# Kernel tuning notes

Hardware: AMD Instinct MI355X
Metric: run time of the kernel (lower is better)

Reference implementation:

```python
import jax, jax.numpy as jnp
import numpy as np

B = 4096        # args.batch_size
M = 2           # n_views (and m in approximate_hsic_zy)
N = B * M       # total rows after torch.cat of views
D = 128         # projector feature dim
GAMMA = 3.0     # args.gamma
SIGMA = 1.0     # Gaussian kernel bandwidth used by compute_gaussian_kernel


def setup_inputs() -> dict:
    key = jax.random.key(0)
    x = jax.random.normal(key, (N, D), dtype=jnp.float32)
    # module applies l2_norm (F.normalize dim=1) before hsic_objective
    feat = x / jnp.maximum(jnp.linalg.norm(x, axis=1, keepdims=True), 1e-12)
    return {"feat": feat}


def _gaussian_kernel(x, y):
    # pairwise squared distances via the GEMM trick, then Gaussian kernel
    sq = (jnp.sum(x * x, axis=1)[:, None]
          + jnp.sum(y * y, axis=1)[None, :]
          - 2.0 * (x @ y.T))
    sq = jnp.maximum(sq, 0.0)
    return jnp.exp(-sq / (2.0 * SIGMA * SIGMA))


def _approximate_hsic_zy(K):
    # labels = cat([arange(B)]*M); labels-equality matrix; exclude diagonal.
    lab = jnp.tile(jnp.arange(B), M)                      # [N]
    eq = (lab[:, None] == lab[None, :]).astype(K.dtype)   # [N,N]
    offdiag = 1.0 - jnp.eye(N, dtype=K.dtype)
    # positives / negatives sums over off-diagonal entries (same math as the
    # boolean-mask view/reshape in torch, expressed as masked reductions)
    pos_sum = jnp.sum(K * eq * offdiag)
    neg_sum = jnp.sum(K * (1.0 - eq) * offdiag)
    term_1 = pos_sum / (B * M * (M - 1))
    term_2 = neg_sum / (B ** 2 * M ** 2)
    term_3 = 1.0 / (M - 1)
    scale = B / (B - 1.0)  # get_label_weights(batch_size) stand-in
    return scale * (term_1 - term_2 - term_3)


def _hsic_regular(K):
    # HSIC(z,z) with doubly-centered kernel: mean(Kc * Kc) since Kx == Ky
    row_m = jnp.mean(K, axis=0, keepdims=True)
    col_m = jnp.mean(K, axis=1, keepdims=True)
    tot_m = jnp.mean(K)
    Kc = K - row_m - col_m + tot_m
    return jnp.mean(Kc * Kc)


def reference(feat):
    K = _gaussian_kernel(feat, feat)          # [N,N] pairwise Gaussian kernel
    hsic_zy = _approximate_hsic_zy(K)
    hsic_zz = _hsic_regular(K)
    return -hsic_zy + GAMMA * jnp.sqrt(hsic_zz)
```

## Files before the change

kernel.cpp:

```cpp
#include <hip/hip_runtime.h>
#include <hip/hip_bf16.h>


using bf16   = __bf16;
using bf16x8 = __attribute__((ext_vector_type(8))) __bf16;
using f32x4  = __attribute__((ext_vector_type(4))) float;

#define N_ROWS 8192
#define LOG2E 1.4426950408889634f

__device__ inline bf16x8 cvt8s(const float4 a, const float4 b, const float s) {
  bf16x8 r;
  r[0] = (__bf16)(a.x * s); r[1] = (__bf16)(a.y * s);
  r[2] = (__bf16)(a.z * s); r[3] = (__bf16)(a.w * s);
  r[4] = (__bf16)(b.x * s); r[5] = (__bf16)(b.y * s);
  r[6] = (__bf16)(b.z * s); r[7] = (__bf16)(b.w * s);
  return r;
}

__global__ __launch_bounds__(256, 2) void gram_kernel(
    const float* __restrict__ feat, float* __restrict__ rpart,
    float* __restrict__ bscal) {
  const int bjc = blockIdx.x, bi = blockIdx.y;
  const int tid = threadIdx.x, lane = tid & 63, w = tid >> 6;
  const int wr = w >> 1, wc = w & 1;
  const int l15 = lane & 15, l4 = lane >> 4;

  __shared__ char  lds_a[32768];
  __shared__ float rbuf[128];
  __shared__ float sS[4], sD[4], sP[4];

  {
    const int rowbase = bi * 128;
#pragma unroll
    for (int i = 0; i < 8; ++i) {
      const int c = tid + i * 256;
      const int row = c >> 4, seg = c & 15;
      const float4* p = (const float4*)(feat + (rowbase + row) * 128 + seg * 8);
      const float4 x0 = p[0], x1 = p[1];
      const int sw = ((row << 8) | (seg << 4)) ^ ((row & 7) << 4);
      *(bf16x8*)(lds_a + sw) = cvt8s(x0, x1, LOG2E);
    }
    if (tid < 128) rbuf[tid] = 0.f;
  }
  __syncthreads();

  float rsum[4][4] = {};
  float s2a = 0.f, s2b = 0.f, pdiag = 0.f, ppos = 0.f;

  float4 bn[4][2];
  {
    const int brow0 = (bjc * 8) * 128 + wc * 64;
#pragma unroll
    for (int f = 0; f < 4; ++f) {
      const float* p = feat + (brow0 + f * 16 + l15) * 128 + l4 * 8;
      bn[f][0] = *(const float4*)p;
      bn[f][1] = *(const float4*)(p + 4);
    }
  }

  for (int t = 0; t < 8; ++t) {
    const int bj = bjc * 8 + t;
    const int brow0 = bj * 128 + wc * 64;

    f32x4 acc[4][4];
#pragma unroll
    for (int fr = 0; fr < 4; ++fr)
#pragma unroll
      for (int fc = 0; fc < 4; ++fc)
#pragma unroll
        for (int e = 0; e < 4; ++e) acc[fr][fc][e] = -LOG2E;

#pragma unroll
    for (int ks = 0; ks < 4; ++ks) {
      bf16x8 bb[4];
#pragma unroll
      for (int f = 0; f < 4; ++f) bb[f] = cvt8s(bn[f][0], bn[f][1], 1.0f);

      if (ks < 3 || t < 7) {
        const int nks = (ks < 3) ? ks + 1 : 0;
        const int nbrow0 = (ks < 3) ? brow0 : brow0 + 128;
#pragma unroll
        for (int f = 0; f < 4; ++f) {
          const float* p =
              feat + (nbrow0 + f * 16 + l15) * 128 + nks * 32 + l4 * 8;
          bn[f][0] = *(const float4*)p;
          bn[f][1] = *(const float4*)(p + 4);
        }
      }

#pragma unroll
      for (int fr = 0; fr < 4; ++fr) {
        const int arow = wr * 64 + fr * 16 + l15;
        const int byte = (arow << 8) + ks * 64 + (l4 << 4);
        const bf16x8 a = *(const bf16x8*)(lds_a + (byte ^ ((arow & 7) << 4)));
#pragma unroll
        for (int fc = 0; fc < 4; ++fc)
          acc[fr][fc] = __builtin_amdgcn_mfma_f32_16x16x32_bf16(
              a, bb[fc], acc[fr][fc], 0, 0, 0);
      }
    }

    const int dt = bj - bi;
    const bool isd = (dt == 0);
    const bool isp = (dt == 32) | (dt == -32);

#pragma unroll
    for (int fr = 0; fr < 4; ++fr) {
#pragma unroll
      for (int fc = 0; fc < 4; ++fc) {
#pragma unroll
        for (int e = 0; e < 4; ++e) {
          const float me = fminf(acc[fr][fc][e], 0.f);
          const float K = exp2f(me);
          if (fc & 1) s2b = fmaf(K, K, s2b); else s2a = fmaf(K, K, s2a);
          rsum[fr][e] += K;
          if (isd | isp) {
            const int rr = wr * 64 + fr * 16 + l4 * 4 + e;
            const int cc = wc * 64 + fc * 16 + l15;
            const float hit = (rr == cc) ? K : 0.f;
            if (isd) pdiag += hit; else ppos += hit;
          }
        }
      }
    }
  }

#pragma unroll
  for (int fr = 0; fr < 4; ++fr) {
#pragma unroll
    for (int e = 0; e < 4; ++e) {
      float r = rsum[fr][e];
      r += __shfl_xor(r, 1);
      r += __shfl_xor(r, 2);
      r += __shfl_xor(r, 4);
      r += __shfl_xor(r, 8);
      if (l15 == 0) atomicAdd(&rbuf[wr * 64 + fr * 16 + l4 * 4 + e], r);
    }
  }
  float s2 = s2a + s2b;
#pragma unroll
  for (int m = 1; m < 64; m <<= 1) {
    s2 += __shfl_xor(s2, m);
    pdiag += __shfl_xor(pdiag, m);
    ppos += __shfl_xor(ppos, m);
  }
  if (lane == 0) { sS[w] = s2; sD[w] = pdiag; sP[w] = ppos; }
  __syncthreads();

  const int slot = bi * 8 + bjc;
  if (tid < 128) rpart[slot * 128 + tid] = rbuf[tid];
  if (tid == 0) {
    bscal[slot * 3 + 0] = sS[0] + sS[1] + sS[2] + sS[3];
    bscal[slot * 3 + 1] = sD[0] + sD[1] + sD[2] + sD[3];
    bscal[slot * 3 + 2] = sP[0] + sP[1] + sP[2] + sP[3];
  }
}

__global__ __launch_bounds__(256) void final_kernel(
    const float* __restrict__ rpart, const float* __restrict__ bscal,
    float* __restrict__ out) {
  const int tid = threadIdx.x, lane = tid & 63, w = tid >> 6;
  double t = 0.0, v2 = 0.0, s2 = 0.0, dg = 0.0, ps = 0.0;
  for (int i = tid; i < N_ROWS; i += 256) {
    const int rb = i >> 7, r = i & 127;
    float s = 0.f;
#pragma unroll
    for (int c = 0; c < 8; ++c) s += rpart[(rb * 8 + c) * 128 + r];
    const double x = (double)s;
    t += x;
    v2 += x * x;
  }
  for (int i = tid; i < 512; i += 256) {
    s2 += (double)bscal[i * 3 + 0];
    dg += (double)bscal[i * 3 + 1];
    ps += (double)bscal[i * 3 + 2];
  }
#pragma unroll
  for (int m = 1; m < 64; m <<= 1) {
    t += __shfl_xor(t, m);
    v2 += __shfl_xor(v2, m);
    s2 += __shfl_xor(s2, m);
    dg += __shfl_xor(dg, m);
    ps += __shfl_xor(ps, m);
  }
  __shared__ double sh[5][4];
  if (lane == 0) {
    sh[0][w] = t; sh[1][w] = v2; sh[2][w] = s2; sh[3][w] = dg; sh[4][w] = ps;
  }
  __syncthreads();
  if (tid == 0) {
    const double T  = sh[0][0] + sh[0][1] + sh[0][2] + sh[0][3];
    const double V2 = sh[1][0] + sh[1][1] + sh[1][2] + sh[1][3];
    const double S2 = sh[2][0] + sh[2][1] + sh[2][2] + sh[2][3];
    const double DG = sh[3][0] + sh[3][1] + sh[3][2] + sh[3][3];
    const double PS = sh[4][0] + sh[4][1] + sh[4][2] + sh[4][3];
    const double Nd = 8192.0, Bd = 4096.0;
    const double hzz = (S2 - (2.0 / Nd) * V2 + (T * T) / (Nd * Nd)) / (Nd * Nd);
    const double neg = (T - DG) - PS;
    const double t1 = PS / 8192.0;
    const double t2 = neg / 67108864.0;
    const double hzy = (Bd / (Bd - 1.0)) * (t1 - t2 - 1.0);
    out[0] = (float)(-hzy + 3.0 * sqrt(fmax(hzz, 0.0)));
  }
}

extern "C" void kernel_launch(void* const* d_in, const int* in_sizes, int n_in,
                              void* d_out, int out_size, void* d_ws,
                              size_t ws_size, hipStream_t stream) {
  (void)in_sizes; (void)n_in; (void)out_size; (void)ws_size;
  const float* feat = (const float*)d_in[0];
  char* ws = (char*)d_ws;
  float* rpart = (float*)ws;
  float* bscal = (float*)(ws + 262144);
  float* out = (float*)d_out;

  gram_kernel<<<dim3(8, 64), 256, 0, stream>>>(feat, rpart, bscal);
  final_kernel<<<1, 256, 0, stream>>>(rpart, bscal, out);
}
```

Before: 137.9 us.

## Pre-convert features to bf16, double gram grid, split final reduction

Adds a prep kernel that converts the fp32 features to bf16 once, so the gram kernel loads half the bytes and skips per-tile conversion. LOG2E is now applied inside the exponent via the hardware exp2 builtin instead of being folded into the A operand. The gram grid grows from 8x64 to 16x64 blocks with 4 column tiles each, giving more parallelism on the many CUs. The single-block final reduction is replaced by a 16-block partial pass plus a tiny combine kernel. The cost is two extra kernel launches and a bf16 workspace round trip.

```diff
diff --git a/kernel.cpp b/kernel.cpp
--- a/kernel.cpp
+++ b/kernel.cpp
@@ -9,17 +9,25 @@
 #define N_ROWS 8192
 #define LOG2E 1.4426950408889634f
 
-__device__ inline bf16x8 cvt8s(const float4 a, const float4 b, const float s) {
+#if __has_builtin(__builtin_amdgcn_exp2f)
+#define EXP2(x) __builtin_amdgcn_exp2f(x)
+#else
+#define EXP2(x) exp2f(x)
+#endif
+
+__global__ __launch_bounds__(256) void prep_kernel(
+    const float* __restrict__ feat, unsigned short* __restrict__ xb) {
+  const int g = blockIdx.x * 256 + threadIdx.x;
+  const float4 a = ((const float4*)feat)[g * 2];
+  const float4 b = ((const float4*)feat)[g * 2 + 1];
   bf16x8 r;
-  r[0] = (__bf16)(a.x * s); r[1] = (__bf16)(a.y * s);
-  r[2] = (__bf16)(a.z * s); r[3] = (__bf16)(a.w * s);
-  r[4] = (__bf16)(b.x * s); r[5] = (__bf16)(b.y * s);
-  r[6] = (__bf16)(b.z * s); r[7] = (__bf16)(b.w * s);
-  return r;
+  r[0] = (__bf16)a.x; r[1] = (__bf16)a.y; r[2] = (__bf16)a.z; r[3] = (__bf16)a.w;
+  r[4] = (__bf16)b.x; r[5] = (__bf16)b.y; r[6] = (__bf16)b.z; r[7] = (__bf16)b.w;
+  ((bf16x8*)xb)[g] = r;
 }
 
 __global__ __launch_bounds__(256, 2) void gram_kernel(
-    const float* __restrict__ feat, float* __restrict__ rpart,
+    const bf16* __restrict__ xb, float* __restrict__ rpart,
     float* __restrict__ bscal) {
   const int bjc = blockIdx.x, bi = blockIdx.y;
   const int tid = threadIdx.x, lane = tid & 63, w = tid >> 6;
@@ -36,10 +44,9 @@
     for (int i = 0; i < 8; ++i) {
       const int c = tid + i * 256;
       const int row = c >> 4, seg = c & 15;
-      const float4* p = (const float4*)(feat + (rowbase + row) * 128 + seg * 8);
-      const float4 x0 = p[0], x1 = p[1];
+      const bf16x8 v = *(const bf16x8*)(xb + (rowbase + row) * 128 + seg * 8);
       const int sw = ((row << 8) | (seg << 4)) ^ ((row & 7) << 4);
-      *(bf16x8*)(lds_a + sw) = cvt8s(x0, x1, LOG2E);
+      *(bf16x8*)(lds_a + sw) = v;
     }
     if (tid < 128) rbuf[tid] = 0.f;
   }
@@ -48,19 +55,17 @@
   float rsum[4][4] = {};
   float s2a = 0.f, s2b = 0.f, pdiag = 0.f, ppos = 0.f;
 
-  float4 bn[4][2];
+  bf16x8 bn[4];
   {
-    const int brow0 = (bjc * 8) * 128 + wc * 64;
-#pragma unroll
-    for (int f = 0; f < 4; ++f) {
-      const float* p = feat + (brow0 + f * 16 + l15) * 128 + l4 * 8;
-      bn[f][0] = *(const float4*)p;
-      bn[f][1] = *(const float4*)(p + 4);
-    }
-  }
-
-  for (int t = 0; t < 8; ++t) {
-    const int bj = bjc * 8 + t;
+    const int brow0 = (bjc * 4) * 128 + wc * 64;
+#pragma unroll
+    for (int f = 0; f < 4; ++f)
+      bn[f] = *(const bf16x8*)(xb + (brow0 + f * 16 + l15) * 128 + l4 * 8);
+  }
+
+#pragma unroll
+  for (int t = 0; t < 4; ++t) {
+    const int bj = bjc * 4 + t;
     const int brow0 = bj * 128 + wc * 64;
 
     f32x4 acc[4][4];
@@ -69,24 +74,21 @@
 #pragma unroll
       for (int fc = 0; fc < 4; ++fc)
 #pragma unroll
-        for (int e = 0; e < 4; ++e) acc[fr][fc][e] = -LOG2E;
+        for (int e = 0; e < 4; ++e) acc[fr][fc][e] = -1.0f;
 
 #pragma unroll
     for (int ks = 0; ks < 4; ++ks) {
       bf16x8 bb[4];
 #pragma unroll
-      for (int f = 0; f < 4; ++f) bb[f] = cvt8s(bn[f][0], bn[f][1], 1.0f);
-
-      if (ks < 3 || t < 7) {
-        const int nks = (ks < 3) ? ks + 1 : 0;
+      for (int f = 0; f < 4; ++f) bb[f] = bn[f];
+
+      if (ks < 3 || t < 3) {
+        const int nks = (ks + 1) & 3;
         const int nbrow0 = (ks < 3) ? brow0 : brow0 + 128;
 #pragma unroll
-        for (int f = 0; f < 4; ++f) {
-          const float* p =
-              feat + (nbrow0 + f * 16 + l15) * 128 + nks * 32 + l4 * 8;
-          bn[f][0] = *(const float4*)p;
-          bn[f][1] = *(const float4*)(p + 4);
-        }
+        for (int f = 0; f < 4; ++f)
+          bn[f] = *(const bf16x8*)(xb + (nbrow0 + f * 16 + l15) * 128 +
+                                   nks * 32 + l4 * 8);
       }
 
 #pragma unroll
@@ -112,7 +114,7 @@
 #pragma unroll
         for (int e = 0; e < 4; ++e) {
           const float me = fminf(acc[fr][fc][e], 0.f);
-          const float K = exp2f(me);
+          const float K = EXP2(me * LOG2E);
           if (fc & 1) s2b = fmaf(K, K, s2b); else s2a = fmaf(K, K, s2a);
           rsum[fr][e] += K;
           if (isd | isp) {
@@ -148,7 +150,7 @@
   if (lane == 0) { sS[w] = s2; sD[w] = pdiag; sP[w] = ppos; }
   __syncthreads();
 
-  const int slot = bi * 8 + bjc;
+  const int slot = bi * 16 + bjc;
   if (tid < 128) rpart[slot * 128 + tid] = rbuf[tid];
   if (tid == 0) {
     bscal[slot * 3 + 0] = sS[0] + sS[1] + sS[2] + sS[3];
@@ -157,24 +159,27 @@
   }
 }
 
-__global__ __launch_bounds__(256) void final_kernel(
+__global__ __launch_bounds__(256) void red1_kernel(
     const float* __restrict__ rpart, const float* __restrict__ bscal,
-    float* __restrict__ out) {
-  const int tid = threadIdx.x, lane = tid & 63, w = tid >> 6;
+    double* __restrict__ gpart) {
+  const int b = blockIdx.x, tid = threadIdx.x, lane = tid & 63, w = tid >> 6;
   double t = 0.0, v2 = 0.0, s2 = 0.0, dg = 0.0, ps = 0.0;
-  for (int i = tid; i < N_ROWS; i += 256) {
-    const int rb = i >> 7, r = i & 127;
+#pragma unroll
+  for (int k = 0; k < 2; ++k) {
+    const int row = b * 512 + k * 256 + tid;
+    const int rb = row >> 7, r = row & 127;
     float s = 0.f;
 #pragma unroll
-    for (int c = 0; c < 8; ++c) s += rpart[(rb * 8 + c) * 128 + r];
+    for (int c = 0; c < 16; ++c) s += rpart[(rb * 16 + c) * 128 + r];
     const double x = (double)s;
     t += x;
     v2 += x * x;
   }
-  for (int i = tid; i < 512; i += 256) {
-    s2 += (double)bscal[i * 3 + 0];
-    dg += (double)bscal[i * 3 + 1];
-    ps += (double)bscal[i * 3 + 2];
+  if (tid < 64) {
+    const int i = b * 64 + tid;
+    s2 = (double)bscal[i * 3 + 0];
+    dg = (double)bscal[i * 3 + 1];
+    ps = (double)bscal[i * 3 + 2];
   }
 #pragma unroll
   for (int m = 1; m < 64; m <<= 1) {
@@ -190,15 +195,38 @@
   }
   __syncthreads();
   if (tid == 0) {
-    const double T  = sh[0][0] + sh[0][1] + sh[0][2] + sh[0][3];
-    const double V2 = sh[1][0] + sh[1][1] + sh[1][2] + sh[1][3];
-    const double S2 = sh[2][0] + sh[2][1] + sh[2][2] + sh[2][3];
-    const double DG = sh[3][0] + sh[3][1] + sh[3][2] + sh[3][3];
-    const double PS = sh[4][0] + sh[4][1] + sh[4][2] + sh[4][3];
+    gpart[b * 5 + 0] = sh[0][0] + sh[0][1] + sh[0][2] + sh[0][3];
+    gpart[b * 5 + 1] = sh[1][0] + sh[1][1] + sh[1][2] + sh[1][3];
+    gpart[b * 5 + 2] = sh[2][0] + sh[2][1] + sh[2][2] + sh[2][3];
+    gpart[b * 5 + 3] = sh[3][0] + sh[3][1] + sh[3][2] + sh[3][3];
+    gpart[b * 5 + 4] = sh[4][0] + sh[4][1] + sh[4][2] + sh[4][3];
+  }
+}
+
+__global__ __launch_bounds__(64) void red2_kernel(
+    const double* __restrict__ gpart, float* __restrict__ out) {
+  const int lane = threadIdx.x;
+  double t = 0.0, v2 = 0.0, s2 = 0.0, dg = 0.0, ps = 0.0;
+  if (lane < 16) {
+    t  = gpart[lane * 5 + 0];
+    v2 = gpart[lane * 5 + 1];
+    s2 = gpart[lane * 5 + 2];
+    dg = gpart[lane * 5 + 3];
+    ps = gpart[lane * 5 + 4];
+  }
+#pragma unroll
+  for (int m = 1; m < 16; m <<= 1) {
+    t += __shfl_xor(t, m);
+    v2 += __shfl_xor(v2, m);
+    s2 += __shfl_xor(s2, m);
+    dg += __shfl_xor(dg, m);
+    ps += __shfl_xor(ps, m);
+  }
+  if (lane == 0) {
     const double Nd = 8192.0, Bd = 4096.0;
-    const double hzz = (S2 - (2.0 / Nd) * V2 + (T * T) / (Nd * Nd)) / (Nd * Nd);
-    const double neg = (T - DG) - PS;
-    const double t1 = PS / 8192.0;
+    const double hzz = (s2 - (2.0 / Nd) * v2 + (t * t) / (Nd * Nd)) / (Nd * Nd);
+    const double neg = (t - dg) - ps;
+    const double t1 = ps / 8192.0;
     const double t2 = neg / 67108864.0;
     const double hzy = (Bd / (Bd - 1.0)) * (t1 - t2 - 1.0);
     out[0] = (float)(-hzy + 3.0 * sqrt(fmax(hzz, 0.0)));
@@ -211,10 +239,14 @@
   (void)in_sizes; (void)n_in; (void)out_size; (void)ws_size;
   const float* feat = (const float*)d_in[0];
   char* ws = (char*)d_ws;
-  float* rpart = (float*)ws;
-  float* bscal = (float*)(ws + 262144);
+  unsigned short* xb = (unsigned short*)ws;
+  float* rpart  = (float*)(ws + 2097152);
+  float* bscal  = (float*)(ws + 2097152 + 524288);
+  double* gpart = (double*)(ws + 2097152 + 524288 + 12288);
   float* out = (float*)d_out;
 
-  gram_kernel<<<dim3(8, 64), 256, 0, stream>>>(feat, rpart, bscal);
-  final_kernel<<<1, 256, 0, stream>>>(rpart, bscal, out);
-}
+  prep_kernel<<<512, 256, 0, stream>>>(feat, xb);
+  gram_kernel<<<dim3(16, 64), 256, 0, stream>>>((const bf16*)xb, rpart, bscal);
+  red1_kernel<<<16, 256, 0, stream>>>(rpart, bscal, gpart);
+  red2_kernel<<<1, 64, 0, stream>>>(gpart, out);
+}
```

New measurement: 138.9 us. Within noise of the previous version (+0.7%).
